# Kernel tuning notes

Hardware: AMD Instinct MI355X
Metric: run time of the kernel (lower is better)

The kernel has to match this reference:

```python
import jax, jax.numpy as jnp
import numpy as np

BS, NS, NCP, NH, C, HID, R = 8, 2048, 8, 8, 128, 128, 128


def rotation_6d_to_matrix(d6):
    a1, a2 = d6[..., :3], d6[..., 3:]
    b1 = a1 / jnp.linalg.norm(a1, axis=-1, keepdims=True)
    b2 = a2 - jnp.sum(b1 * a2, axis=-1, keepdims=True) * b1
    b2 = b2 / jnp.linalg.norm(b2, axis=-1, keepdims=True)
    b3 = jnp.cross(b1, b2)
    return jnp.stack([b1, b2, b3], axis=-2)  # (..., 3, 3), rows b1,b2,b3


def _sample_plane(plane, uv):
    # plane: (B,C,R,R); uv: (B,N,2) in [0,1]; uv[...,0]->width, uv[...,1]->height
    Rr = plane.shape[-1]
    x = jnp.clip(uv[..., 0], 0.0, 1.0) * (Rr - 1)
    y = jnp.clip(uv[..., 1], 0.0, 1.0) * (Rr - 1)
    x0 = jnp.floor(x); y0 = jnp.floor(y)
    wx = x - x0; wy = y - y0
    x0i = x0.astype(jnp.int32); y0i = y0.astype(jnp.int32)
    x1i = jnp.minimum(x0i + 1, Rr - 1); y1i = jnp.minimum(y0i + 1, Rr - 1)
    gb = jax.vmap(lambda p, yi, xi: p[:, yi, xi])  # per-batch gather -> (C,N)
    f00 = gb(plane, y0i, x0i); f01 = gb(plane, y0i, x1i)
    f10 = gb(plane, y1i, x0i); f11 = gb(plane, y1i, x1i)
    wx = wx[:, None, :]; wy = wy[:, None, :]
    f = f00 * (1 - wx) * (1 - wy) + f01 * wx * (1 - wy) + f10 * (1 - wx) * wy + f11 * wx * wy
    return jnp.transpose(f, (0, 2, 1))  # (B,N,C)


def triplane_sample(p, pxz, pxy, pyz):
    # p: (B,N,3) in [0,1]^3; sum of bilinear samples from the three planes
    return (_sample_plane(pxz, p[..., jnp.array([0, 2])])
            + _sample_plane(pxy, p[..., jnp.array([0, 1])])
            + _sample_plane(pyz, p[..., jnp.array([1, 2])]))


def setup_inputs() -> dict:
    key = jax.random.key(0)
    ks = jax.random.split(key, 10)
    s = 1.0 / np.sqrt(C)
    return {
        "query_pos": jax.random.uniform(ks[0], (BS, NS, 9), dtype=jnp.float32),
        "plane_xz": jax.random.normal(ks[1], (BS, C, R, R), dtype=jnp.float32),
        "plane_xy": jax.random.normal(ks[2], (BS, C, R, R), dtype=jnp.float32),
        "plane_yz": jax.random.normal(ks[3], (BS, C, R, R), dtype=jnp.float32),
        "control_points": jax.random.normal(ks[4], (NCP, 3), dtype=jnp.float32) * 0.05,
        "W_v": jax.random.normal(ks[5], (C, HID), dtype=jnp.float32) * s,
        "b_v": jnp.zeros((HID,), jnp.float32),
        "W_w": jax.random.normal(ks[6], (C, NCP * NH), dtype=jnp.float32) * s,
        "b_w": jnp.zeros((NCP * NH,), jnp.float32),
        "W_o": jax.random.normal(ks[7], (HID, C), dtype=jnp.float32) * s,
        "b_o": jnp.zeros((C,), jnp.float32),
    }


def reference(query_pos, plane_xz, plane_xy, plane_yz, control_points,
              W_v, b_v, W_w, b_w, W_o, b_o):
    bs, ns, _ = query_pos.shape
    q_ori = query_pos[..., 3:]
    q_pos = query_pos[..., :3]
    feature = triplane_sample(q_pos, plane_xz, plane_xy, plane_yz)  # (bs,ns,C)
    rot = rotation_6d_to_matrix(q_ori)  # (bs,ns,3,3)
    # rotate control points: einsum('bnpd,bngd->bngp') with cp broadcast over (bs,ns)
    cp = jnp.einsum('bnpd,gd->bngp', rot, control_points)  # (bs,ns,ncp,3)
    anchor = q_pos[:, :, None, :] + cp  # (bs,ns,ncp,3)
    sf = triplane_sample(anchor.reshape(bs, ns * NCP, 3), plane_xz, plane_xy, plane_yz)
    sf = sf.reshape(bs * ns, NCP, C)  # head dim in torch code is a pure repeat
    feat = feature.reshape(bs * ns, C)
    w = (feat @ W_w + b_w).reshape(bs * ns, NCP, NH)  # (B,ncp,heads)
    vbase = sf @ W_v + b_v  # (B,ncp,hid); identical across repeated head dim
    # torch: (v * weights).sum((1,2)) with v_t[b,i,j,k]=vbase[b,j,k], w[b,i,j]
    out = jnp.einsum('bjk,bij->bk', vbase, w)  # (B,hid)
    out = out @ W_o + b_o
    out = out + feat
    return out.reshape(bs, ns, -1)
```

## Files before the change

### kernel.cpp

```cpp
#include <hip/hip_runtime.h>
#include <hip/hip_fp16.h>
#include <math.h>

constexpr int BS  = 8;
constexpr int NS  = 2048;
constexpr int NCP = 8;
constexpr int NH  = 8;
constexpr int C   = 128;
constexpr int HID = 128;
constexpr int RR  = 128;

constexpr int QPB = 8;
constexpr int VEC = 4;

constexpr int NPOS = RR * RR;
constexpr size_t PLE = (size_t)BS * NPOS * C;

constexpr int NBLK_T = 384;
constexpr int QPOS   = 2048;
constexpr int SPOS   = 256;
constexpr int LROWH  = 260;

using f4v = __attribute__((ext_vector_type(4))) float;

struct F4 { float x, y, z, w; };
__device__ __forceinline__ F4 f4add(F4 a, F4 b) {
    return F4{a.x + b.x, a.y + b.y, a.z + b.z, a.w + b.w};
}
__device__ __forceinline__ F4 f4fma(F4 acc, float s, F4 v) {
    return F4{fmaf(s, v.x, acc.x), fmaf(s, v.y, acc.y),
              fmaf(s, v.z, acc.z), fmaf(s, v.w, acc.w)};
}
__device__ __forceinline__ F4 cvt4(int2 r) {
    __half2 h0 = *reinterpret_cast<__half2*>(&r.x);
    __half2 h1 = *reinterpret_cast<__half2*>(&r.y);
    float2 f0 = __half22float2(h0);
    float2 f1 = __half22float2(h1);
    return F4{f0.x, f0.y, f1.x, f1.y};
}

__global__ __launch_bounds__(256) void trans_prep_k(
    const float* __restrict__ pxz, const float* __restrict__ pxy,
    const float* __restrict__ pyz, __half* __restrict__ dst,
    const float* __restrict__ Wv, const float* __restrict__ bv,
    const float* __restrict__ Ww, const float* __restrict__ bw,
    const float* __restrict__ Wo,
    float* __restrict__ Wf, float* __restrict__ bf,
    float* __restrict__ Ww2, float* __restrict__ bw2)
{
    __shared__ __half lh[64 * LROWH];

    const int bid = blockIdx.x;
    const int t   = threadIdx.x;

    if (bid >= NBLK_T) {
        const int k = bid - NBLK_T;
        const int c = t;
        if (c >= 128) return;
        if (k < 128) {
            float acc = 0.f;
            #pragma unroll 8
            for (int j = 0; j < 128; ++j) acc += Wv[k * 128 + j] * Wo[j * 128 + c];
            Wf[k * 128 + c] = acc;
        } else if (k == 128) {
            float acc = 0.f;
            #pragma unroll 8
            for (int j = 0; j < 128; ++j) acc += bv[j] * Wo[j * 128 + c];
            bf[c] = acc;
        } else {
            float s[NH];
            #pragma unroll
            for (int h = 0; h < NH; ++h) s[h] = 0.f;
            #pragma unroll
            for (int i = 0; i < NCP; ++i)
                #pragma unroll
                for (int h = 0; h < NH; ++h) s[h] += Ww[c * (NCP * NH) + i * NH + h];
            #pragma unroll
            for (int h = 0; h < NH; ++h) Ww2[c * NH + h] = s[h];
            if (c < NH) {
                float tt = 0.f;
                #pragma unroll
                for (int i = 0; i < NCP; ++i) tt += bw[i * NH + c];
                bw2[c] = tt;
            }
        }
        return;
    }

    const int b   = bid & 7;
    const int rem = bid >> 3;
    const int pl  = rem >> 4;
    const int r2  = rem & 15;
    const int cg  = r2 >> 3;
    const int q   = r2 & 7;
    const int ch0 = cg * 64;
    const int pos0 = q * QPOS;

    const float* src = (pl == 0 ? pxz : (pl == 1 ? pxy : pyz))
                       + (size_t)b * C * NPOS;
    __half* d = dst + (size_t)(pl * BS + b) * ((size_t)NPOS * C);

    const int g32  = t >> 5;
    const int l32  = t & 31;

    f4v v[16];
    #pragma unroll
    for (int i = 0; i < 16; ++i) {
        const int chL  = g32 * 8 + (i >> 1);
        const int posL = ((i & 1) << 7) + (l32 << 2);
        v[i] = __builtin_nontemporal_load(reinterpret_cast<const f4v*>(
                   src + (size_t)(ch0 + chL) * NPOS + pos0 + posL));
    }

    #pragma unroll
    for (int sc = 0; sc < 8; ++sc) {
        __syncthreads();

        #pragma unroll
        for (int i = 0; i < 16; ++i) {
            const int chL  = g32 * 8 + (i >> 1);
            const int posL = ((i & 1) << 7) + (l32 << 2);
            __half2 h0 = __floats2half2_rn(v[i][0], v[i][1]);
            __half2 h1 = __floats2half2_rn(v[i][2], v[i][3]);
            uint2 w;
            w.x = *reinterpret_cast<unsigned*>(&h0);
            w.y = *reinterpret_cast<unsigned*>(&h1);
            *reinterpret_cast<uint2*>(&lh[chL * LROWH + posL]) = w;
        }

        f4v nv[16];
        if (sc < 7) {
            #pragma unroll
            for (int i = 0; i < 16; ++i) {
                const int chL  = g32 * 8 + (i >> 1);
                const int posL = ((i & 1) << 7) + (l32 << 2);
                nv[i] = __builtin_nontemporal_load(reinterpret_cast<const f4v*>(
                            src + (size_t)(ch0 + chL) * NPOS + pos0
                                + (sc + 1) * SPOS + posL));
            }
        }
        __syncthreads();

        {
            const int p = t;
            unsigned w[32];
            #pragma unroll
            for (int k = 0; k < 32; ++k) {
                const unsigned lo = *reinterpret_cast<const unsigned short*>(
                                        &lh[(2 * k) * LROWH + p]);
                const unsigned hi = *reinterpret_cast<const unsigned short*>(
                                        &lh[(2 * k + 1) * LROWH + p]);
                w[k] = lo | (hi << 16);
            }
            __half* drow = d + (size_t)(pos0 + sc * SPOS + p) * C + ch0;
            #pragma unroll
            for (int j = 0; j < 8; ++j) {
                *reinterpret_cast<uint4*>(drow + j * 8) =
                    make_uint4(w[4 * j], w[4 * j + 1], w[4 * j + 2], w[4 * j + 3]);
            }
        }

        #pragma unroll
        for (int i = 0; i < 16; ++i) v[i] = nv[i];
    }
}

__device__ __forceinline__ F4 samp(const __half* __restrict__ base, float u, float v)
{
    float x = fminf(fmaxf(u, 0.f), 1.f) * (float)(RR - 1);
    float y = fminf(fmaxf(v, 0.f), 1.f) * (float)(RR - 1);
    float x0f = floorf(x), y0f = floorf(y);
    float wx = x - x0f, wy = y - y0f;
    int x0 = (int)x0f, y0 = (int)y0f;
    int x1 = min(x0 + 1, RR - 1), y1 = min(y0 + 1, RR - 1);
    int r0 = y0 << 14, r1 = y1 << 14, cc0 = x0 << 7, cc1 = x1 << 7;
    int2 a00 = *reinterpret_cast<const int2*>(base + r0 + cc0);
    int2 a01 = *reinterpret_cast<const int2*>(base + r0 + cc1);
    int2 a10 = *reinterpret_cast<const int2*>(base + r1 + cc0);
    int2 a11 = *reinterpret_cast<const int2*>(base + r1 + cc1);
    float w00 = (1.f - wx) * (1.f - wy), w01 = wx * (1.f - wy);
    float w10 = (1.f - wx) * wy,         w11 = wx * wy;
    F4 f00 = cvt4(a00), f01 = cvt4(a01), f10 = cvt4(a10), f11 = cvt4(a11);
    F4 r;
    r.x = f00.x * w00 + f01.x * w01 + f10.x * w10 + f11.x * w11;
    r.y = f00.y * w00 + f01.y * w01 + f10.y * w10 + f11.y * w11;
    r.z = f00.z * w00 + f01.z * w01 + f10.z * w10 + f11.z * w11;
    r.w = f00.w * w00 + f01.w * w01 + f10.w * w10 + f11.w * w11;
    return r;
}

__global__ __launch_bounds__(256) void attn_k(
    const float* __restrict__ qpos,
    const __half* __restrict__ planes,
    const float* __restrict__ cpts,
    const float* __restrict__ Ww2, const float* __restrict__ bw2,
    const float* __restrict__ Wf,  const float* __restrict__ bf,
    const float* __restrict__ bo,
    float* __restrict__ out)
{
    const int nb   = gridDim.x;
    const int cpx  = nb >> 3;
    const int sbid = (blockIdx.x & 7) * cpx + (blockIdx.x >> 3);

    const int tid  = threadIdx.x;
    const int ql   = tid >> 5;
    const int lane = tid & 31;
    const int c4   = lane * VEC;
    const int q    = sbid * QPB + ql;
    const int b    = q >> 11;

    const float* qp = qpos + (size_t)q * 9;
    const float px = qp[0], py = qp[1], pz = qp[2];
    const float a1x = qp[3], a1y = qp[4], a1z = qp[5];
    const float a2x = qp[6], a2y = qp[7], a2z = qp[8];

    float inv = 1.f / sqrtf(a1x * a1x + a1y * a1y + a1z * a1z);
    float b1x = a1x * inv, b1y = a1y * inv, b1z = a1z * inv;
    float dd  = b1x * a2x + b1y * a2y + b1z * a2z;
    float b2x = a2x - dd * b1x, b2y = a2y - dd * b1y, b2z = a2z - dd * b1z;
    inv = 1.f / sqrtf(b2x * b2x + b2y * b2y + b2z * b2z);
    b2x *= inv; b2y *= inv; b2z *= inv;
    float b3x = b1y * b2z - b1z * b2y;
    float b3y = b1z * b2x - b1x * b2z;
    float b3z = b1x * b2y - b1y * b2x;

    const __half* Pxz = planes + (size_t)b * ((size_t)NPOS * C) + c4;
    const __half* Pxy = Pxz + PLE;
    const __half* Pyz = Pxy + PLE;

    F4 feat = f4add(f4add(samp(Pxz, px, pz), samp(Pxy, px, py)), samp(Pyz, py, pz));

    float p[NH];
    #pragma unroll
    for (int h = 0; h < NH; ++h) p[h] = 0.f;
    {
        const float* wr = Ww2 + c4 * NH;
        const float fv[VEC] = {feat.x, feat.y, feat.z, feat.w};
        #pragma unroll
        for (int i = 0; i < VEC; ++i)
            #pragma unroll
            for (int h = 0; h < NH; ++h) p[h] += fv[i] * wr[i * NH + h];
    }
    #pragma unroll
    for (int off = 16; off >= 1; off >>= 1)
        #pragma unroll
        for (int h = 0; h < NH; ++h) p[h] += __shfl_xor(p[h], off);

    float ws[NH], Ssum = 0.f;
    #pragma unroll
    for (int h = 0; h < NH; ++h) { ws[h] = p[h] + bw2[h]; Ssum += ws[h]; }

    F4 comb = {0.f, 0.f, 0.f, 0.f};
    #pragma unroll 2
    for (int g = 0; g < NCP; ++g) {
        float cx = cpts[g * 3 + 0], cy = cpts[g * 3 + 1], cz = cpts[g * 3 + 2];
        float ax = px + b1x * cx + b1y * cy + b1z * cz;
        float ay = py + b2x * cx + b2y * cy + b2z * cz;
        float az = pz + b3x * cx + b3y * cy + b3z * cz;
        F4 s = f4add(f4add(samp(Pxz, ax, az), samp(Pxy, ax, ay)), samp(Pyz, ay, az));
        comb = f4fma(comb, ws[g], s);
    }

    __shared__ float sComb[QPB][C];
    __shared__ float sFeat[QPB][C];
    __shared__ float sSum[QPB];
    *reinterpret_cast<float4*>(&sComb[ql][c4]) = make_float4(comb.x, comb.y, comb.z, comb.w);
    *reinterpret_cast<float4*>(&sFeat[ql][c4]) = make_float4(feat.x, feat.y, feat.z, feat.w);
    if (lane == 0) sSum[ql] = Ssum;
    __syncthreads();

    const int c  = tid & 127;
    const int q0 = (tid >> 7) * 4;
    float acc[4];
    const float bfc = bf[c], boc = bo[c];
    #pragma unroll
    for (int j = 0; j < 4; ++j)
        acc[j] = sSum[q0 + j] * bfc + boc + sFeat[q0 + j][c];
    #pragma unroll 4
    for (int k = 0; k < C; ++k) {
        float wf = Wf[k * C + c];
        #pragma unroll
        for (int j = 0; j < 4; ++j) acc[j] += sComb[q0 + j][k] * wf;
    }
    #pragma unroll
    for (int j = 0; j < 4; ++j)
        out[(size_t)(sbid * QPB + q0 + j) * C + c] = acc[j];
}

extern "C" void kernel_launch(void* const* d_in, const int* in_sizes, int n_in,
                              void* d_out, int out_size, void* d_ws, size_t ws_size,
                              hipStream_t stream)
{
    const float* qpos = (const float*)d_in[0];
    const float* pxz  = (const float*)d_in[1];
    const float* pxy  = (const float*)d_in[2];
    const float* pyz  = (const float*)d_in[3];
    const float* cpts = (const float*)d_in[4];
    const float* Wv   = (const float*)d_in[5];
    const float* bv   = (const float*)d_in[6];
    const float* Ww   = (const float*)d_in[7];
    const float* bw   = (const float*)d_in[8];
    const float* Wo   = (const float*)d_in[9];
    const float* bo   = (const float*)d_in[10];
    float* out = (float*)d_out;

    __half* plh = (__half*)d_ws;
    float*  wsf = (float*)((char*)d_ws + 3 * PLE * sizeof(__half));
    float* Wf  = wsf;
    float* bf  = Wf + C * HID;
    float* Ww2 = bf + C;
    float* bw2 = Ww2 + C * NH;

    hipLaunchKernelGGL(trans_prep_k, dim3(NBLK_T + 130), dim3(256), 0, stream,
                       pxz, pxy, pyz, plh, Wv, bv, Ww, bw, Wo, Wf, bf, Ww2, bw2);

    hipLaunchKernelGGL(attn_k, dim3(BS * NS / QPB), dim3(256), 0, stream,
                       qpos, plh, cpts, Ww2, bw2, Wf, bf, bo, out);
}
```

Before: 133.0 us.

## Batch all triplane gathers per plane and retile fp16 transpose kernel

The attention kernel now computes all nine sample positions (query plus eight anchors) up front and issues all 36 gathers for each plane before doing any interpolation. This exposes more memory-level parallelism, where before the gathers were serialized per sample. The transpose/convert kernel launches four times as many blocks, each covering fewer positions, and its write phase is remapped so consecutive threads store adjacent 16-byte chunks of the same row, giving coalesced writes. The cost is much higher register pressure in the attention kernel, which may reduce occupancy.

```diff
diff --git a/kernel.cpp b/kernel.cpp
--- a/kernel.cpp
+++ b/kernel.cpp
@@ -16,8 +16,8 @@
 constexpr int NPOS = RR * RR;
 constexpr size_t PLE = (size_t)BS * NPOS * C;
 
-constexpr int NBLK_T = 384;
-constexpr int QPOS   = 2048;
+constexpr int NBLK_T = 1536;
+constexpr int QPOS   = 512;
 constexpr int SPOS   = 256;
 constexpr int LROWH  = 260;
 
@@ -87,13 +87,13 @@
         return;
     }
 
-    const int b   = bid & 7;
-    const int rem = bid >> 3;
-    const int pl  = rem >> 4;
-    const int r2  = rem & 15;
-    const int cg  = r2 >> 3;
-    const int q   = r2 & 7;
-    const int ch0 = cg * 64;
+    const int b    = bid & 7;
+    const int rem  = bid >> 3;
+    const int pl   = rem >> 6;
+    const int r2   = rem & 63;
+    const int cg   = r2 >> 5;
+    const int q    = r2 & 31;
+    const int ch0  = cg * 64;
     const int pos0 = q * QPOS;
 
     const float* src = (pl == 0 ? pxz : (pl == 1 ? pxy : pyz))
@@ -113,7 +113,7 @@
     }
 
     #pragma unroll
-    for (int sc = 0; sc < 8; ++sc) {
+    for (int sc = 0; sc < 2; ++sc) {
         __syncthreads();
 
         #pragma unroll
@@ -129,7 +129,7 @@
         }
 
         f4v nv[16];
-        if (sc < 7) {
+        if (sc < 1) {
             #pragma unroll
             for (int i = 0; i < 16; ++i) {
                 const int chL  = g32 * 8 + (i >> 1);
@@ -141,52 +141,27 @@
         }
         __syncthreads();
 
-        {
-            const int p = t;
-            unsigned w[32];
-            #pragma unroll
-            for (int k = 0; k < 32; ++k) {
+        const int cbase = (t & 7) * 8;
+        #pragma unroll
+        for (int j = 0; j < 8; ++j) {
+            const int p = 32 * j + (t >> 3);
+            unsigned w[4];
+            #pragma unroll
+            for (int k = 0; k < 4; ++k) {
                 const unsigned lo = *reinterpret_cast<const unsigned short*>(
-                                        &lh[(2 * k) * LROWH + p]);
+                                        &lh[(cbase + 2 * k) * LROWH + p]);
                 const unsigned hi = *reinterpret_cast<const unsigned short*>(
-                                        &lh[(2 * k + 1) * LROWH + p]);
+                                        &lh[(cbase + 2 * k + 1) * LROWH + p]);
                 w[k] = lo | (hi << 16);
             }
-            __half* drow = d + (size_t)(pos0 + sc * SPOS + p) * C + ch0;
-            #pragma unroll
-            for (int j = 0; j < 8; ++j) {
-                *reinterpret_cast<uint4*>(drow + j * 8) =
-                    make_uint4(w[4 * j], w[4 * j + 1], w[4 * j + 2], w[4 * j + 3]);
-            }
+            *reinterpret_cast<uint4*>(
+                d + (size_t)(pos0 + sc * SPOS + p) * C + ch0 + cbase) =
+                make_uint4(w[0], w[1], w[2], w[3]);
         }
 
         #pragma unroll
         for (int i = 0; i < 16; ++i) v[i] = nv[i];
     }
-}
-
-__device__ __forceinline__ F4 samp(const __half* __restrict__ base, float u, float v)
-{
-    float x = fminf(fmaxf(u, 0.f), 1.f) * (float)(RR - 1);
-    float y = fminf(fmaxf(v, 0.f), 1.f) * (float)(RR - 1);
-    float x0f = floorf(x), y0f = floorf(y);
-    float wx = x - x0f, wy = y - y0f;
-    int x0 = (int)x0f, y0 = (int)y0f;
-    int x1 = min(x0 + 1, RR - 1), y1 = min(y0 + 1, RR - 1);
-    int r0 = y0 << 14, r1 = y1 << 14, cc0 = x0 << 7, cc1 = x1 << 7;
-    int2 a00 = *reinterpret_cast<const int2*>(base + r0 + cc0);
-    int2 a01 = *reinterpret_cast<const int2*>(base + r0 + cc1);
-    int2 a10 = *reinterpret_cast<const int2*>(base + r1 + cc0);
-    int2 a11 = *reinterpret_cast<const int2*>(base + r1 + cc1);
-    float w00 = (1.f - wx) * (1.f - wy), w01 = wx * (1.f - wy);
-    float w10 = (1.f - wx) * wy,         w11 = wx * wy;
-    F4 f00 = cvt4(a00), f01 = cvt4(a01), f10 = cvt4(a10), f11 = cvt4(a11);
-    F4 r;
-    r.x = f00.x * w00 + f01.x * w01 + f10.x * w10 + f11.x * w11;
-    r.y = f00.y * w00 + f01.y * w01 + f10.y * w10 + f11.y * w11;
-    r.z = f00.z * w00 + f01.z * w01 + f10.z * w10 + f11.z * w11;
-    r.w = f00.w * w00 + f01.w * w01 + f10.w * w10 + f11.w * w11;
-    return r;
 }
 
 __global__ __launch_bounds__(256) void attn_k(
@@ -224,11 +199,61 @@
     float b3y = b1z * b2x - b1x * b2z;
     float b3z = b1x * b2y - b1y * b2x;
 
+    float posx[9], posy[9], posz[9];
+    posx[0] = px; posy[0] = py; posz[0] = pz;
+    #pragma unroll
+    for (int g = 0; g < NCP; ++g) {
+        float cx = cpts[g * 3 + 0], cy = cpts[g * 3 + 1], cz = cpts[g * 3 + 2];
+        posx[g + 1] = px + b1x * cx + b1y * cy + b1z * cz;
+        posy[g + 1] = py + b2x * cx + b2y * cy + b2z * cz;
+        posz[g + 1] = pz + b3x * cx + b3y * cy + b3z * cz;
+    }
+
     const __half* Pxz = planes + (size_t)b * ((size_t)NPOS * C) + c4;
     const __half* Pxy = Pxz + PLE;
     const __half* Pyz = Pxy + PLE;
 
-    F4 feat = f4add(f4add(samp(Pxz, px, pz), samp(Pxy, px, py)), samp(Pyz, py, pz));
+    F4 fs[9];
+    #pragma unroll
+    for (int k = 0; k < 9; ++k) fs[k] = F4{0.f, 0.f, 0.f, 0.f};
+
+    #pragma unroll
+    for (int pl = 0; pl < 3; ++pl) {
+        const __half* P = (pl == 0) ? Pxz : ((pl == 1) ? Pxy : Pyz);
+        int2  dd4[9][4];
+        float wxa[9], wya[9];
+        #pragma unroll
+        for (int k = 0; k < 9; ++k) {
+            float u = (pl == 2) ? posy[k] : posx[k];
+            float v = (pl == 1) ? posy[k] : posz[k];
+            float x = fminf(fmaxf(u, 0.f), 1.f) * (float)(RR - 1);
+            float y = fminf(fmaxf(v, 0.f), 1.f) * (float)(RR - 1);
+            float x0f = floorf(x), y0f = floorf(y);
+            wxa[k] = x - x0f; wya[k] = y - y0f;
+            int x0 = (int)x0f, y0 = (int)y0f;
+            int x1 = min(x0 + 1, RR - 1), y1 = min(y0 + 1, RR - 1);
+            const __half* r0p = P + (y0 << 14);
+            const __half* r1p = P + (y1 << 14);
+            dd4[k][0] = *reinterpret_cast<const int2*>(r0p + (x0 << 7));
+            dd4[k][1] = *reinterpret_cast<const int2*>(r0p + (x1 << 7));
+            dd4[k][2] = *reinterpret_cast<const int2*>(r1p + (x0 << 7));
+            dd4[k][3] = *reinterpret_cast<const int2*>(r1p + (x1 << 7));
+        }
+        #pragma unroll
+        for (int k = 0; k < 9; ++k) {
+            float wx = wxa[k], wy = wya[k];
+            float w00 = (1.f - wx) * (1.f - wy), w01 = wx * (1.f - wy);
+            float w10 = (1.f - wx) * wy,         w11 = wx * wy;
+            F4 f00 = cvt4(dd4[k][0]), f01 = cvt4(dd4[k][1]);
+            F4 f10 = cvt4(dd4[k][2]), f11 = cvt4(dd4[k][3]);
+            fs[k].x += f00.x * w00 + f01.x * w01 + f10.x * w10 + f11.x * w11;
+            fs[k].y += f00.y * w00 + f01.y * w01 + f10.y * w10 + f11.y * w11;
+            fs[k].z += f00.z * w00 + f01.z * w01 + f10.z * w10 + f11.z * w11;
+            fs[k].w += f00.w * w00 + f01.w * w01 + f10.w * w10 + f11.w * w11;
+        }
+    }
+
+    const F4 feat = fs[0];
 
     float p[NH];
     #pragma unroll
@@ -251,15 +276,8 @@
     for (int h = 0; h < NH; ++h) { ws[h] = p[h] + bw2[h]; Ssum += ws[h]; }
 
     F4 comb = {0.f, 0.f, 0.f, 0.f};
-    #pragma unroll 2
-    for (int g = 0; g < NCP; ++g) {
-        float cx = cpts[g * 3 + 0], cy = cpts[g * 3 + 1], cz = cpts[g * 3 + 2];
-        float ax = px + b1x * cx + b1y * cy + b1z * cz;
-        float ay = py + b2x * cx + b2y * cy + b2z * cz;
-        float az = pz + b3x * cx + b3y * cy + b3z * cz;
-        F4 s = f4add(f4add(samp(Pxz, ax, az), samp(Pxy, ax, ay)), samp(Pyz, ay, az));
-        comb = f4fma(comb, ws[g], s);
-    }
+    #pragma unroll
+    for (int g = 0; g < NCP; ++g) comb = f4fma(comb, ws[g], fs[g + 1]);
 
     __shared__ float sComb[QPB][C];
     __shared__ float sFeat[QPB][C];
```

New measurement: 136.1 us. 1.02x slower.

## Bin queries spatially and split transpose into more blocks for locality

Applied to the files above, without the earlier changes.

Adds three small kernels (histogram, scan, scatter) that sort queries into 64 spatial bins per batch, and makes the attention kernel process queries in this permuted order, writing outputs back to their original indices. Nearby queries then sample nearby plane texels, which should improve cache hit rates for the random gathers. The plane transpose kernel is also split into four times as many blocks, each covering fewer positions, and its LDS readback is restructured so each thread writes one 16-byte chunk per row. The cost is three extra launches plus atomics on global counters.

```diff
diff --git a/kernel.cpp b/kernel.cpp
--- a/kernel.cpp
+++ b/kernel.cpp
@@ -16,10 +16,13 @@
 constexpr int NPOS = RR * RR;
 constexpr size_t PLE = (size_t)BS * NPOS * C;
 
-constexpr int NBLK_T = 384;
-constexpr int QPOS   = 2048;
+constexpr int NBLK_T = 1536;
+constexpr int QPOS   = 512;
 constexpr int SPOS   = 256;
 constexpr int LROWH  = 260;
+
+constexpr int NBINS  = 64;
+constexpr int NQ     = BS * NS;
 
 using f4v = __attribute__((ext_vector_type(4))) float;
 
@@ -46,13 +49,18 @@
     const float* __restrict__ Ww, const float* __restrict__ bw,
     const float* __restrict__ Wo,
     float* __restrict__ Wf, float* __restrict__ bf,
-    float* __restrict__ Ww2, float* __restrict__ bw2)
+    float* __restrict__ Ww2, float* __restrict__ bw2,
+    unsigned* __restrict__ hist)
 {
     __shared__ __half lh[64 * LROWH];
 
     const int bid = blockIdx.x;
     const int t   = threadIdx.x;
 
+    if (bid >= NBLK_T + 130) {
+        hist[(bid - (NBLK_T + 130)) * 256 + t] = 0u;
+        return;
+    }
     if (bid >= NBLK_T) {
         const int k = bid - NBLK_T;
         const int c = t;
@@ -87,13 +95,13 @@
         return;
     }
 
-    const int b   = bid & 7;
-    const int rem = bid >> 3;
-    const int pl  = rem >> 4;
-    const int r2  = rem & 15;
-    const int cg  = r2 >> 3;
-    const int q   = r2 & 7;
-    const int ch0 = cg * 64;
+    const int b    = bid & 7;
+    const int rem  = bid >> 3;
+    const int pl   = rem >> 6;
+    const int r2   = rem & 63;
+    const int cg   = r2 >> 5;
+    const int q    = r2 & 31;
+    const int ch0  = cg * 64;
     const int pos0 = q * QPOS;
 
     const float* src = (pl == 0 ? pxz : (pl == 1 ? pxy : pyz))
@@ -113,7 +121,7 @@
     }
 
     #pragma unroll
-    for (int sc = 0; sc < 8; ++sc) {
+    for (int sc = 0; sc < 2; ++sc) {
         __syncthreads();
 
         #pragma unroll
@@ -129,7 +137,7 @@
         }
 
         f4v nv[16];
-        if (sc < 7) {
+        if (sc < 1) {
             #pragma unroll
             for (int i = 0; i < 16; ++i) {
                 const int chL  = g32 * 8 + (i >> 1);
@@ -141,28 +149,72 @@
         }
         __syncthreads();
 
-        {
-            const int p = t;
-            unsigned w[32];
-            #pragma unroll
-            for (int k = 0; k < 32; ++k) {
+        const int cbase = (t & 7) * 8;
+        #pragma unroll
+        for (int j = 0; j < 8; ++j) {
+            const int p = 32 * j + (t >> 3);
+            unsigned w[4];
+            #pragma unroll
+            for (int k = 0; k < 4; ++k) {
                 const unsigned lo = *reinterpret_cast<const unsigned short*>(
-                                        &lh[(2 * k) * LROWH + p]);
+                                        &lh[(cbase + 2 * k) * LROWH + p]);
                 const unsigned hi = *reinterpret_cast<const unsigned short*>(
-                                        &lh[(2 * k + 1) * LROWH + p]);
+                                        &lh[(cbase + 2 * k + 1) * LROWH + p]);
                 w[k] = lo | (hi << 16);
             }
-            __half* drow = d + (size_t)(pos0 + sc * SPOS + p) * C + ch0;
-            #pragma unroll
-            for (int j = 0; j < 8; ++j) {
-                *reinterpret_cast<uint4*>(drow + j * 8) =
-                    make_uint4(w[4 * j], w[4 * j + 1], w[4 * j + 2], w[4 * j + 3]);
-            }
+            *reinterpret_cast<uint4*>(
+                d + (size_t)(pos0 + sc * SPOS + p) * C + ch0 + cbase) =
+                make_uint4(w[0], w[1], w[2], w[3]);
         }
 
         #pragma unroll
         for (int i = 0; i < 16; ++i) v[i] = nv[i];
     }
+}
+
+__device__ __forceinline__ int bin_of(const float* qp) {
+    int bx = min((int)(fminf(fmaxf(qp[0], 0.f), 1.f) * 4.f), 3);
+    int by = min((int)(fminf(fmaxf(qp[1], 0.f), 1.f) * 4.f), 3);
+    int bz = min((int)(fminf(fmaxf(qp[2], 0.f), 1.f) * 4.f), 3);
+    return (bz << 4) | (by << 2) | bx;
+}
+
+__global__ __launch_bounds__(256) void bin_count_k(
+    const float* __restrict__ qpos, unsigned* __restrict__ hist,
+    unsigned* __restrict__ binid)
+{
+    const int q = blockIdx.x * 256 + threadIdx.x;
+    const float* qp = qpos + (size_t)q * 9;
+    const int bin = ((q >> 11) << 6) | bin_of(qp);
+    binid[q] = (unsigned)bin;
+    atomicAdd(&hist[bin], 1u);
+}
+
+__global__ __launch_bounds__(512) void scan_k(
+    const unsigned* __restrict__ hist, unsigned* __restrict__ cursor)
+{
+    __shared__ unsigned s[512];
+    const int t = threadIdx.x;
+    const unsigned h = hist[t];
+    s[t] = h;
+    __syncthreads();
+    #pragma unroll
+    for (int off = 1; off < 512; off <<= 1) {
+        unsigned u = (t >= off) ? s[t - off] : 0u;
+        __syncthreads();
+        s[t] += u;
+        __syncthreads();
+    }
+    cursor[t] = s[t] - h;
+}
+
+__global__ __launch_bounds__(256) void scatter_k(
+    const unsigned* __restrict__ binid, unsigned* __restrict__ cursor,
+    unsigned* __restrict__ perm)
+{
+    const int q = blockIdx.x * 256 + threadIdx.x;
+    const unsigned pos = atomicAdd(&cursor[binid[q]], 1u);
+    perm[pos] = (unsigned)q;
 }
 
 __device__ __forceinline__ F4 samp(const __half* __restrict__ base, float u, float v)
@@ -193,6 +245,7 @@
     const float* __restrict__ qpos,
     const __half* __restrict__ planes,
     const float* __restrict__ cpts,
+    const unsigned* __restrict__ perm,
     const float* __restrict__ Ww2, const float* __restrict__ bw2,
     const float* __restrict__ Wf,  const float* __restrict__ bf,
     const float* __restrict__ bo,
@@ -206,8 +259,11 @@
     const int ql   = tid >> 5;
     const int lane = tid & 31;
     const int c4   = lane * VEC;
-    const int q    = sbid * QPB + ql;
+    const int q    = (int)perm[sbid * QPB + ql];
     const int b    = q >> 11;
+
+    __shared__ unsigned sQ[QPB];
+    if (lane == 0) sQ[ql] = (unsigned)q;
 
     const float* qp = qpos + (size_t)q * 9;
     const float px = qp[0], py = qp[1], pz = qp[2];
@@ -284,7 +340,7 @@
     }
     #pragma unroll
     for (int j = 0; j < 4; ++j)
-        out[(size_t)(sbid * QPB + q0 + j) * C + c] = acc[j];
+        out[(size_t)sQ[q0 + j] * C + c] = acc[j];
 }
 
 extern "C" void kernel_launch(void* const* d_in, const int* in_sizes, int n_in,
@@ -310,10 +366,19 @@
     float* bf  = Wf + C * HID;
     float* Ww2 = bf + C;
     float* bw2 = Ww2 + C * NH;
-
-    hipLaunchKernelGGL(trans_prep_k, dim3(NBLK_T + 130), dim3(256), 0, stream,
-                       pxz, pxy, pyz, plh, Wv, bv, Ww, bw, Wo, Wf, bf, Ww2, bw2);
-
-    hipLaunchKernelGGL(attn_k, dim3(BS * NS / QPB), dim3(256), 0, stream,
-                       qpos, plh, cpts, Ww2, bw2, Wf, bf, bo, out);
-}
+    unsigned* hist   = (unsigned*)(bw2 + NH);
+    unsigned* cursor = hist + 512;
+    unsigned* binid  = cursor + 512;
+    unsigned* perm   = binid + NQ;
+
+    hipLaunchKernelGGL(trans_prep_k, dim3(NBLK_T + 132), dim3(256), 0, stream,
+                       pxz, pxy, pyz, plh, Wv, bv, Ww, bw, Wo, Wf, bf, Ww2, bw2,
+                       hist);
+    hipLaunchKernelGGL(bin_count_k, dim3(NQ / 256), dim3(256), 0, stream,
+                       qpos, hist, binid);
+    hipLaunchKernelGGL(scan_k, dim3(1), dim3(512), 0, stream, hist, cursor);
+    hipLaunchKernelGGL(scatter_k, dim3(NQ / 256), dim3(256), 0, stream,
+                       binid, cursor, perm);
+    hipLaunchKernelGGL(attn_k, dim3(NQ / QPB), dim3(256), 0, stream,
+                       qpos, plh, cpts, perm, Ww2, bw2, Wf, bf, bo, out);
+}
```

After: 124.9 us. 6.1% less time.
